# Performance work log

Measured on AMD Instinct MI355X. Metric: run time of the kernel, lower is better.

## Reference

```python
import jax, jax.numpy as jnp
import numpy as np

N, H, CIN, C, G = 50000, 16, 256, 256, 8
CPG = C // G          # 32 channels per group
CR = C // 4           # delta MLP hidden (delta_reduction=4)

def _lrelu(x):
    return jax.nn.leaky_relu(x, 0.1)

def setup_inputs() -> dict:
    key = jax.random.key(0)
    ks = jax.random.split(key, 16)
    def lin(k, fin, fout):
        return jax.random.normal(k, (fin, fout), jnp.float32) / np.sqrt(fin)
    return {
        'q_pts': jax.random.normal(ks[0], (N, 3), jnp.float32),
        's_pts': jax.random.normal(ks[1], (N, 3), jnp.float32),
        's_feats': jax.random.normal(ks[2], (N, CIN), jnp.float32),
        'neighb_inds': jax.random.randint(ks[3], (N, H), 0, N, jnp.int64),
        'Wq': lin(ks[4], CIN, C), 'bq': jnp.zeros((C,), jnp.float32),
        'Wk': lin(ks[5], CIN, C), 'bk': jnp.zeros((C,), jnp.float32),
        'Wv': lin(ks[6], CIN, C), 'bv': jnp.zeros((C,), jnp.float32),
        'Wd1': lin(ks[7], 3, CR), 'bd1': jnp.zeros((CR,), jnp.float32),
        'Wd2': lin(ks[8], CR, C), 'bd2': jnp.zeros((C,), jnp.float32),
        'Wa1': lin(ks[9], C, CPG), 'ba1': jnp.zeros((CPG,), jnp.float32),
        'Wa2': lin(ks[10], CPG, CPG), 'ba2': jnp.zeros((CPG,), jnp.float32),
    }

def reference(q_pts, s_pts, s_feats, neighb_inds,
              Wq, bq, Wk, bk, Wv, bv,
              Wd1, bd1, Wd2, bd2, Wa1, ba1, Wa2, ba2):
    # q/k/v projections  (N, C)
    v = s_feats @ Wv + bv
    k = s_feats @ Wk + bk
    q = s_feats @ Wq + bq
    # gather neighbor features (all indices < N, shadow mask is a no-op)
    nv = v[neighb_inds]                 # (N, H, C)
    nk = k[neighb_inds]                 # (N, H, C)
    # relative positions (torch.no_grad in source)
    rel = s_pts[neighb_inds] - q_pts[:, None, :]   # (N, H, 3)
    # delta MLP: 3 -> C/4 -> C (UnaryBlock + Linear, norm='none')
    geom = _lrelu(rel @ Wd1 + bd1) @ Wd2 + bd2     # (N, H, C)
    # geom_mode='sub': v-branch and qk-branch both subtract geom encodings
    nv = nv - geom
    # source always enters strided branch (s_pts padded before the check);
    # stride_mode='nearest' -> q feature of the first neighbor
    qf = q[neighb_inds[:, 0]]                      # (N, C)
    qk = qf[:, None, :] - nk - geom                # (N, H, C)
    # alpha MLP: NormBlock(id) + act, Linear C->CpG + act, Linear CpG->CpG
    a = _lrelu(qk)
    a = _lrelu(a @ Wa1 + ba1)
    a = a @ Wa2 + ba2                              # (N, H, CpG)
    attn = jax.nn.softmax(a, axis=1)               # softmax over neighbors
    # grouped weighted aggregation: C split as (CpG, G), attn broadcast over G
    out = (nv.reshape(N, H, CPG, G) * attn[..., None]).sum(axis=1)
    return out.reshape(N, C)
```

## Files before the change

kernel.cpp:

```cpp
#include <hip/hip_runtime.h>
#include <cstdint>
#include <cstddef>

#define N_PTS 50000
#define H 16
#define CIN 256
#define C 256
#define CPG 32
#define CR 64

typedef short bf16x8 __attribute__((ext_vector_type(8)));
typedef float f32x4 __attribute__((ext_vector_type(4)));

__device__ __forceinline__ unsigned short f2bf(float f) {
    unsigned int u = __float_as_uint(f);
    u += 0x7fff + ((u >> 16) & 1);
    return (unsigned short)(u >> 16);
}
__device__ __forceinline__ float bf2f(unsigned short s) {
    return __uint_as_float(((unsigned int)s) << 16);
}

__global__ __launch_bounds__(256) void prep_all(
    const float* __restrict__ feats,
    const float* __restrict__ Wq, const float* __restrict__ Wk,
    const float* __restrict__ Wv,
    const float* __restrict__ Wd2, const float* __restrict__ Wa1,
    const float* __restrict__ Wa2,
    unsigned short* __restrict__ A_bf16,
    unsigned short* __restrict__ gemmFrags,
    unsigned short* __restrict__ attnFrags)
{
    int bid = blockIdx.x;
    if (bid < 6250) {
        size_t i = ((size_t)bid * 256 + threadIdx.x) * 8;
        float4 f0 = *(const float4*)&feats[i];
        float4 f1 = *(const float4*)&feats[i + 4];
        unsigned short t[8] = {f2bf(f0.x), f2bf(f0.y), f2bf(f0.z), f2bf(f0.w),
                               f2bf(f1.x), f2bf(f1.y), f2bf(f1.z), f2bf(f1.w)};
        *(bf16x8*)&A_bf16[i] = *(bf16x8*)t;
    } else if (bid < 6346) {
        int t = (bid - 6250) * 256 + threadIdx.x;
        int lane = t & 63;
        int f = t >> 6;
        int ntg = f % 48;
        const float* W = ntg < 16 ? Wq : (ntg < 32 ? Wk : Wv);
        int colc = (ntg & 15) * 16 + (lane & 15);
        int row0 = (f / 48) * 32 + ((lane >> 4) << 3);
        unsigned short tmp[8];
        #pragma unroll
        for (int j = 0; j < 8; ++j) tmp[j] = f2bf(W[(size_t)(row0 + j) * 256 + colc]);
        *(bf16x8*)&gemmFrags[(size_t)t * 8] = *(bf16x8*)tmp;
    } else {
        int t = (bid - 6346) * 256 + threadIdx.x;
        if (t >= 3200) return;
        const float* W; int Nc, NT, loc, base;
        if (t < 2048)      { W = Wd2; Nc = 256; NT = 16; loc = t;        base = 0; }
        else if (t < 3072) { W = Wa1; Nc = 32;  NT = 2;  loc = t - 2048; base = 16384; }
        else               { W = Wa2; Nc = 32;  NT = 2;  loc = t - 3072; base = 24576; }
        int f = loc >> 6, lane = loc & 63;
        int kt = f / NT, nt = f - kt * NT;
        int colc = nt * 16 + (lane & 15);
        int row0 = kt * 32 + ((lane >> 4) << 3);
        unsigned short tmp[8];
        #pragma unroll
        for (int j = 0; j < 8; ++j) tmp[j] = f2bf(W[(size_t)(row0 + j) * Nc + colc]);
        *(bf16x8*)&attnFrags[(size_t)(base + loc * 8)] = *(bf16x8*)tmp;
    }
}

__global__ __launch_bounds__(256) void qkv_gemm_mfma(
    const unsigned short* __restrict__ A,
    const unsigned short* __restrict__ wfrags,
    const float* __restrict__ bq, const float* __restrict__ bk,
    const float* __restrict__ bv, unsigned short* __restrict__ out)
{
    __shared__ unsigned short s_a[128 * 40];
    const int tid = threadIdx.x;
    const int lane = tid & 63, wave = tid >> 6;
    const int quad = lane >> 4, col16 = lane & 15;
    const int bx = blockIdx.x, by = blockIdx.y;

    f32x4 acc[2][8] = {};
    const int mrow = tid >> 1, half = tid & 1;
    const int gm = by * 128 + mrow;

    for (int kt = 0; kt < 8; ++kt) {
        bf16x8 a0 = {0,0,0,0,0,0,0,0}, a1 = a0;
        if (gm < N_PTS) {
            const unsigned short* src = &A[(size_t)gm * 256 + kt * 32 + half * 16];
            a0 = *(const bf16x8*)src;
            a1 = *(const bf16x8*)(src + 8);
        }
        __syncthreads();
        *(bf16x8*)&s_a[mrow * 40 + half * 16]     = a0;
        *(bf16x8*)&s_a[mrow * 40 + half * 16 + 8] = a1;
        __syncthreads();
        bf16x8 af0 = *(bf16x8*)&s_a[(wave * 32 + col16) * 40 + quad * 8];
        bf16x8 af1 = *(bf16x8*)&s_a[(wave * 32 + 16 + col16) * 40 + quad * 8];
        #pragma unroll
        for (int nt = 0; nt < 8; ++nt) {
            bf16x8 bf = *(const bf16x8*)&wfrags[(((size_t)kt * 48 + bx * 8 + nt) * 64 + lane) * 8];
            acc[0][nt] = __builtin_amdgcn_mfma_f32_16x16x32_bf16(af0, bf, acc[0][nt], 0, 0, 0);
            acc[1][nt] = __builtin_amdgcn_mfma_f32_16x16x32_bf16(af1, bf, acc[1][nt], 0, 0, 0);
        }
    }

    const int mode = bx >> 1;
    const float* bias = mode == 0 ? bq : (mode == 1 ? bk : bv);
    #pragma unroll
    for (int nt = 0; nt < 8; ++nt) {
        int cIn = (bx & 1) * 128 + nt * 16 + col16;
        float bb = bias[cIn];
        int pos = mode == 0 ? cIn : (256 + 2 * cIn + (mode == 2 ? 1 : 0));
        #pragma unroll
        for (int mt = 0; mt < 2; ++mt) {
            #pragma unroll
            for (int r = 0; r < 4; ++r) {
                int row = by * 128 + wave * 32 + mt * 16 + quad * 4 + r;
                if (row < N_PTS)
                    out[(size_t)row * 768 + pos] = f2bf(acc[mt][nt][r] + bb);
            }
        }
    }
}

#define D1S 72
#define PGS 66
#define QKS 264
#define A1S 40
#define A2S 33

__global__ __launch_bounds__(256, 3) void attn_mfma(
    const unsigned short* __restrict__ qkv,
    const float* __restrict__ q_pts, const float* __restrict__ s_pts,
    const int* __restrict__ nbr,
    const float* __restrict__ Wd1, const float* __restrict__ bd1,
    const float* __restrict__ bd2,
    const unsigned short* __restrict__ frags,
    const float* __restrict__ ba1, const float* __restrict__ ba2,
    float* __restrict__ out)
{
    __shared__ unsigned short s_d1[H * D1S];
    __shared__ float          s_pg[4 * H * PGS];
    __shared__ unsigned short s_qk[H * QKS];
    __shared__ unsigned short s_a1[H * A1S];
    __shared__ float          s_a2[H * A2S];
    __shared__ float          s_rel[4][H][3];
    __shared__ int            s_idx[4][H];

    const int tid = threadIdx.x;
    const int lane = tid & 63, wave = tid >> 6;
    const int quad = lane >> 4, col = lane & 15;
    const int n0 = blockIdx.x * 4;
    const int c = tid;

    if (tid < 64) {
        int pp = tid >> 4, hh = tid & 15;
        int idx = nbr[(size_t)(n0 + pp) * H + hh];
        s_idx[pp][hh] = idx;
        #pragma unroll
        for (int x = 0; x < 3; ++x)
            s_rel[pp][hh][x] = s_pts[(size_t)idx * 3 + x] - q_pts[(size_t)(n0 + pp) * 3 + x];
    }

    const float w1x = Wd1[lane], w1y = Wd1[64 + lane], w1z = Wd1[128 + lane];
    const float b1 = bd1[lane];
    const float b2 = bd2[c];
    bf16x8 wd2f[2][4];
    #pragma unroll
    for (int t = 0; t < 4; ++t) {
        wd2f[0][t] = *(const bf16x8*)&frags[((size_t)((0 * 16 + wave * 4 + t) * 64 + lane)) * 8];
        wd2f[1][t] = *(const bf16x8*)&frags[((size_t)((1 * 16 + wave * 4 + t) * 64 + lane)) * 8];
    }
    bf16x8 wa1f[8];
    bf16x8 wa2f = {0,0,0,0,0,0,0,0};
    if (wave < 2) {
        #pragma unroll
        for (int kt = 0; kt < 8; ++kt)
            wa1f[kt] = *(const bf16x8*)&frags[16384 + ((size_t)((kt * 2 + wave) * 64 + lane)) * 8];
        wa2f = *(const bf16x8*)&frags[24576 + ((size_t)(wave * 64 + lane)) * 8];
    }
    __syncthreads();

    float* pg = &s_pg[wave * (H * PGS)];

    for (int p = 0; p < 4; ++p) {
        const int n = n0 + p;

        #pragma unroll
        for (int pass = 0; pass < 4; ++pass) {
            int h = pass * 4 + wave;
            float v = b1 + s_rel[p][h][0] * w1x + s_rel[p][h][1] * w1y + s_rel[p][h][2] * w1z;
            s_d1[h * D1S + lane] = f2bf(fmaxf(v, 0.1f * v));
        }
        __syncthreads();

        unsigned int u[H];
        #pragma unroll
        for (int h = 0; h < H; ++h)
            u[h] = *(const unsigned int*)&qkv[(size_t)s_idx[p][h] * 768 + 256 + 2 * c];
        float qf = bf2f(qkv[(size_t)s_idx[p][0] * 768 + c]);

        {
            bf16x8 ga = *(bf16x8*)&s_d1[col * D1S + quad * 8];
            bf16x8 gb = *(bf16x8*)&s_d1[col * D1S + 32 + quad * 8];
            #pragma unroll
            for (int t = 0; t < 4; ++t) {
                f32x4 acc = {0.f, 0.f, 0.f, 0.f};
                acc = __builtin_amdgcn_mfma_f32_16x16x32_bf16(ga, wd2f[0][t], acc, 0, 0, 0);
                acc = __builtin_amdgcn_mfma_f32_16x16x32_bf16(gb, wd2f[1][t], acc, 0, 0, 0);
                #pragma unroll
                for (int rr = 0; rr < 4; ++rr)
                    pg[(quad * 4 + rr) * PGS + t * 16 + col] = acc[rr];
            }
        }

        float vg[H];
        #pragma unroll
        for (int h = 0; h < H; ++h) {
            float g = pg[h * PGS + lane] + b2;
            float nk = __uint_as_float(u[h] << 16);
            float nv = __uint_as_float(u[h] & 0xffff0000u);
            vg[h] = nv - g;
            float tq = qf - nk - g;
            s_qk[h * QKS + c] = f2bf(fmaxf(tq, 0.1f * tq));
        }
        __syncthreads();

        if (wave < 2) {
            f32x4 acc = {0.f, 0.f, 0.f, 0.f};
            #pragma unroll
            for (int kt = 0; kt < 8; ++kt) {
                bf16x8 a = *(bf16x8*)&s_qk[col * QKS + kt * 32 + quad * 8];
                acc = __builtin_amdgcn_mfma_f32_16x16x32_bf16(a, wa1f[kt], acc, 0, 0, 0);
            }
            int j = wave * 16 + col;
            float bb = ba1[j];
            #pragma unroll
            for (int rr = 0; rr < 4; ++rr) {
                float v = acc[rr] + bb;
                s_a1[(quad * 4 + rr) * A1S + j] = f2bf(fmaxf(v, 0.1f * v));
            }
        }
        __syncthreads();

        if (wave < 2) {
            bf16x8 aa = *(bf16x8*)&s_a1[col * A1S + quad * 8];
            f32x4 acc = {0.f, 0.f, 0.f, 0.f};
            acc = __builtin_amdgcn_mfma_f32_16x16x32_bf16(aa, wa2f, acc, 0, 0, 0);
            int j = wave * 16 + col;
            float bb = ba2[j];
            #pragma unroll
            for (int rr = 0; rr < 4; ++rr)
                s_a2[(quad * 4 + rr) * A2S + j] = acc[rr] + bb;
        }
        __syncthreads();

        if (wave == 0) {
            int j = lane & 31, hb = (lane >> 5) * 8;
            float vals[8];
            float mx = -1e30f;
            #pragma unroll
            for (int i = 0; i < 8; ++i) {
                vals[i] = s_a2[(hb + i) * A2S + j];
                mx = fmaxf(mx, vals[i]);
            }
            mx = fmaxf(mx, __shfl_xor(mx, 32));
            float sum = 0.f;
            #pragma unroll
            for (int i = 0; i < 8; ++i) { vals[i] = __expf(vals[i] - mx); sum += vals[i]; }
            sum += __shfl_xor(sum, 32);
            float inv = 1.f / sum;
            #pragma unroll
            for (int i = 0; i < 8; ++i) s_a2[(hb + i) * A2S + j] = vals[i] * inv;
        }
        __syncthreads();

        float o = 0.f;
        const int aj = c >> 3;
        #pragma unroll
        for (int h = 0; h < H; ++h) o += vg[h] * s_a2[h * A2S + aj];
        out[(size_t)n * C + c] = o;
    }
}


extern "C" void kernel_launch(void* const* d_in, const int* in_sizes, int n_in,
                              void* d_out, int out_size, void* d_ws, size_t ws_size,
                              hipStream_t stream) {
    const float* q_pts   = (const float*)d_in[0];
    const float* s_pts   = (const float*)d_in[1];
    const float* s_feats = (const float*)d_in[2];
    const int*   nbr     = (const int*)d_in[3];
    const float* Wq  = (const float*)d_in[4];
    const float* bq  = (const float*)d_in[5];
    const float* Wk  = (const float*)d_in[6];
    const float* bk  = (const float*)d_in[7];
    const float* Wv  = (const float*)d_in[8];
    const float* bv  = (const float*)d_in[9];
    const float* Wd1 = (const float*)d_in[10];
    const float* bd1 = (const float*)d_in[11];
    const float* Wd2 = (const float*)d_in[12];
    const float* bd2 = (const float*)d_in[13];
    const float* Wa1 = (const float*)d_in[14];
    const float* ba1 = (const float*)d_in[15];
    const float* Wa2 = (const float*)d_in[16];
    const float* ba2 = (const float*)d_in[17];

    float* out = (float*)d_out;
    char* ws = (char*)d_ws;
    unsigned short* A_bf16    = (unsigned short*)(ws);
    unsigned short* qkvb      = (unsigned short*)(ws + 25600000);
    unsigned short* attnFrags = (unsigned short*)(ws + 102400000);
    unsigned short* gemmFrags = (unsigned short*)(ws + 102451200);

    prep_all<<<6359, 256, 0, stream>>>(s_feats, Wq, Wk, Wv, Wd2, Wa1, Wa2,
                                       A_bf16, gemmFrags, attnFrags);

    dim3 g1(6, (N_PTS + 127) / 128);
    qkv_gemm_mfma<<<g1, 256, 0, stream>>>(A_bf16, gemmFrags, bq, bk, bv, qkvb);

    attn_mfma<<<(N_PTS / 4), 256, 0, stream>>>(qkvb, q_pts, s_pts, nbr,
                                               Wd1, bd1, bd2, attnFrags,
                                               ba1, ba2, out);
}
```

Before: 404.1 us.

## Double-buffer QKV GEMM loads, prefetch neighbor gathers, and merge alpha MLP stages

The QKV GEMM now double-buffers the A tile in shared memory, prefetching the next k-slice while MFMAs run, and drops one barrier per iteration. K and V columns are interleaved per block so each thread writes packed 32-bit k|v pairs. In the attention kernel, the delta-MLP first layer is computed for all four points up front, the neighbor k/v gathers for the next point are issued before the current softmax/aggregation, and the second alpha layer plus softmax run in a single wave, removing a barrier. This adds register and shared-memory pressure, which may reduce occupancy.

```diff
diff --git a/kernel.cpp b/kernel.cpp
--- a/kernel.cpp
+++ b/kernel.cpp
@@ -75,7 +75,7 @@
     const float* __restrict__ bq, const float* __restrict__ bk,
     const float* __restrict__ bv, unsigned short* __restrict__ out)
 {
-    __shared__ unsigned short s_a[128 * 40];
+    __shared__ unsigned short s_a[2][128 * 40];
     const int tid = threadIdx.x;
     const int lane = tid & 63, wave = tid >> 6;
     const int quad = lane >> 4, col16 = lane & 15;
@@ -84,43 +84,75 @@
     f32x4 acc[2][8] = {};
     const int mrow = tid >> 1, half = tid & 1;
     const int gm = by * 128 + mrow;
-
+    const bool valid = gm < N_PTS;
+    const unsigned short* arow = &A[(size_t)gm * 256 + half * 16];
+
+    {
+        bf16x8 pa0 = {0,0,0,0,0,0,0,0}, pa1 = pa0;
+        if (valid) { pa0 = *(const bf16x8*)arow; pa1 = *(const bf16x8*)(arow + 8); }
+        *(bf16x8*)&s_a[0][mrow * 40 + half * 16]     = pa0;
+        *(bf16x8*)&s_a[0][mrow * 40 + half * 16 + 8] = pa1;
+    }
+
+    #pragma unroll
     for (int kt = 0; kt < 8; ++kt) {
-        bf16x8 a0 = {0,0,0,0,0,0,0,0}, a1 = a0;
-        if (gm < N_PTS) {
-            const unsigned short* src = &A[(size_t)gm * 256 + kt * 32 + half * 16];
-            a0 = *(const bf16x8*)src;
-            a1 = *(const bf16x8*)(src + 8);
+        bf16x8 na0 = {0,0,0,0,0,0,0,0}, na1 = na0;
+        if (kt < 7 && valid) {
+            const unsigned short* src = arow + (kt + 1) * 32;
+            na0 = *(const bf16x8*)src;
+            na1 = *(const bf16x8*)(src + 8);
         }
         __syncthreads();
-        *(bf16x8*)&s_a[mrow * 40 + half * 16]     = a0;
-        *(bf16x8*)&s_a[mrow * 40 + half * 16 + 8] = a1;
-        __syncthreads();
-        bf16x8 af0 = *(bf16x8*)&s_a[(wave * 32 + col16) * 40 + quad * 8];
-        bf16x8 af1 = *(bf16x8*)&s_a[(wave * 32 + 16 + col16) * 40 + quad * 8];
+        const unsigned short* buf = s_a[kt & 1];
+        bf16x8 af0 = *(const bf16x8*)&buf[(wave * 32 + col16) * 40 + quad * 8];
+        bf16x8 af1 = *(const bf16x8*)&buf[(wave * 32 + 16 + col16) * 40 + quad * 8];
         #pragma unroll
         for (int nt = 0; nt < 8; ++nt) {
-            bf16x8 bf = *(const bf16x8*)&wfrags[(((size_t)kt * 48 + bx * 8 + nt) * 64 + lane) * 8];
+            int ntg = (bx < 2) ? (bx * 8 + nt)
+                               : (nt < 4 ? 16 + (bx - 2) * 4 + nt
+                                         : 32 + (bx - 2) * 4 + (nt - 4));
+            bf16x8 bf = *(const bf16x8*)&wfrags[(((size_t)kt * 48 + ntg) * 64 + lane) * 8];
             acc[0][nt] = __builtin_amdgcn_mfma_f32_16x16x32_bf16(af0, bf, acc[0][nt], 0, 0, 0);
             acc[1][nt] = __builtin_amdgcn_mfma_f32_16x16x32_bf16(af1, bf, acc[1][nt], 0, 0, 0);
         }
-    }
-
-    const int mode = bx >> 1;
-    const float* bias = mode == 0 ? bq : (mode == 1 ? bk : bv);
-    #pragma unroll
-    for (int nt = 0; nt < 8; ++nt) {
-        int cIn = (bx & 1) * 128 + nt * 16 + col16;
-        float bb = bias[cIn];
-        int pos = mode == 0 ? cIn : (256 + 2 * cIn + (mode == 2 ? 1 : 0));
-        #pragma unroll
-        for (int mt = 0; mt < 2; ++mt) {
-            #pragma unroll
-            for (int r = 0; r < 4; ++r) {
-                int row = by * 128 + wave * 32 + mt * 16 + quad * 4 + r;
-                if (row < N_PTS)
-                    out[(size_t)row * 768 + pos] = f2bf(acc[mt][nt][r] + bb);
-            }
+        if (kt < 7) {
+            unsigned short* nbuf = s_a[(kt + 1) & 1];
+            *(bf16x8*)&nbuf[mrow * 40 + half * 16]     = na0;
+            *(bf16x8*)&nbuf[mrow * 40 + half * 16 + 8] = na1;
+        }
+    }
+
+    if (bx < 2) {
+        #pragma unroll
+        for (int nt = 0; nt < 8; ++nt) {
+            int cIn = bx * 128 + nt * 16 + col16;
+            float bb = bq[cIn];
+            #pragma unroll
+            for (int mt = 0; mt < 2; ++mt)
+                #pragma unroll
+                for (int r = 0; r < 4; ++r) {
+                    int row = by * 128 + wave * 32 + mt * 16 + quad * 4 + r;
+                    if (row < N_PTS)
+                        out[(size_t)row * 768 + cIn] = f2bf(acc[mt][nt][r] + bb);
+                }
+        }
+    } else {
+        unsigned int* out32 = (unsigned int*)out;
+        #pragma unroll
+        for (int t = 0; t < 4; ++t) {
+            int cIn = (bx - 2) * 64 + t * 16 + col16;
+            float kb = bk[cIn], vb = bv[cIn];
+            #pragma unroll
+            for (int mt = 0; mt < 2; ++mt)
+                #pragma unroll
+                for (int r = 0; r < 4; ++r) {
+                    int row = by * 128 + wave * 32 + mt * 16 + quad * 4 + r;
+                    if (row < N_PTS) {
+                        unsigned int kk = f2bf(acc[mt][t][r] + kb);
+                        unsigned int vv = f2bf(acc[mt][t + 4][r] + vb);
+                        out32[(size_t)row * 384 + 128 + cIn] = kk | (vv << 16);
+                    }
+                }
         }
     }
 }
@@ -141,7 +173,7 @@
     const float* __restrict__ ba1, const float* __restrict__ ba2,
     float* __restrict__ out)
 {
-    __shared__ unsigned short s_d1[H * D1S];
+    __shared__ unsigned short s_d1a[4 * H * D1S];
     __shared__ float          s_pg[4 * H * PGS];
     __shared__ unsigned short s_qk[H * QKS];
     __shared__ unsigned short s_a1[H * A1S];
@@ -174,37 +206,42 @@
         wd2f[1][t] = *(const bf16x8*)&frags[((size_t)((1 * 16 + wave * 4 + t) * 64 + lane)) * 8];
     }
     bf16x8 wa1f[8];
-    bf16x8 wa2f = {0,0,0,0,0,0,0,0};
+    bf16x8 wa2f[2] = {{0,0,0,0,0,0,0,0}, {0,0,0,0,0,0,0,0}};
     if (wave < 2) {
         #pragma unroll
         for (int kt = 0; kt < 8; ++kt)
             wa1f[kt] = *(const bf16x8*)&frags[16384 + ((size_t)((kt * 2 + wave) * 64 + lane)) * 8];
-        wa2f = *(const bf16x8*)&frags[24576 + ((size_t)(wave * 64 + lane)) * 8];
+    }
+    if (wave == 0) {
+        wa2f[0] = *(const bf16x8*)&frags[24576 + ((size_t)(0 * 64 + lane)) * 8];
+        wa2f[1] = *(const bf16x8*)&frags[24576 + ((size_t)(1 * 64 + lane)) * 8];
     }
     __syncthreads();
 
+    #pragma unroll
+    for (int pass = 0; pass < 16; ++pass) {
+        int hp = pass * 4 + wave;
+        int p = hp >> 4, h = hp & 15;
+        float v = b1 + s_rel[p][h][0] * w1x + s_rel[p][h][1] * w1y + s_rel[p][h][2] * w1z;
+        s_d1a[hp * D1S + lane] = f2bf(fmaxf(v, 0.1f * v));
+    }
+    __syncthreads();
+
     float* pg = &s_pg[wave * (H * PGS)];
+
+    unsigned int u[H];
+    #pragma unroll
+    for (int h = 0; h < H; ++h)
+        u[h] = *(const unsigned int*)&qkv[(size_t)s_idx[0][h] * 768 + 256 + 2 * c];
+    float qf = bf2f(qkv[(size_t)s_idx[0][0] * 768 + c]);
 
     for (int p = 0; p < 4; ++p) {
         const int n = n0 + p;
 
-        #pragma unroll
-        for (int pass = 0; pass < 4; ++pass) {
-            int h = pass * 4 + wave;
-            float v = b1 + s_rel[p][h][0] * w1x + s_rel[p][h][1] * w1y + s_rel[p][h][2] * w1z;
-            s_d1[h * D1S + lane] = f2bf(fmaxf(v, 0.1f * v));
-        }
-        __syncthreads();
-
-        unsigned int u[H];
-        #pragma unroll
-        for (int h = 0; h < H; ++h)
-            u[h] = *(const unsigned int*)&qkv[(size_t)s_idx[p][h] * 768 + 256 + 2 * c];
-        float qf = bf2f(qkv[(size_t)s_idx[p][0] * 768 + c]);
-
         {
-            bf16x8 ga = *(bf16x8*)&s_d1[col * D1S + quad * 8];
-            bf16x8 gb = *(bf16x8*)&s_d1[col * D1S + 32 + quad * 8];
+            const unsigned short* d1p = &s_d1a[p * H * D1S];
+            bf16x8 ga = *(const bf16x8*)&d1p[col * D1S + quad * 8];
+            bf16x8 gb = *(const bf16x8*)&d1p[col * D1S + 32 + quad * 8];
             #pragma unroll
             for (int t = 0; t < 4; ++t) {
                 f32x4 acc = {0.f, 0.f, 0.f, 0.f};
@@ -245,19 +282,25 @@
         }
         __syncthreads();
 
-        if (wave < 2) {
+        if (p < 3) {
+            #pragma unroll
+            for (int h = 0; h < H; ++h)
+                u[h] = *(const unsigned int*)&qkv[(size_t)s_idx[p + 1][h] * 768 + 256 + 2 * c];
+            qf = bf2f(qkv[(size_t)s_idx[p + 1][0] * 768 + c]);
+        }
+
+        if (wave == 0) {
             bf16x8 aa = *(bf16x8*)&s_a1[col * A1S + quad * 8];
-            f32x4 acc = {0.f, 0.f, 0.f, 0.f};
-            acc = __builtin_amdgcn_mfma_f32_16x16x32_bf16(aa, wa2f, acc, 0, 0, 0);
-            int j = wave * 16 + col;
-            float bb = ba2[j];
-            #pragma unroll
-            for (int rr = 0; rr < 4; ++rr)
-                s_a2[(quad * 4 + rr) * A2S + j] = acc[rr] + bb;
-        }
-        __syncthreads();
-
-        if (wave == 0) {
+            #pragma unroll
+            for (int nt = 0; nt < 2; ++nt) {
+                f32x4 acc = {0.f, 0.f, 0.f, 0.f};
+                acc = __builtin_amdgcn_mfma_f32_16x16x32_bf16(aa, wa2f[nt], acc, 0, 0, 0);
+                int j = nt * 16 + col;
+                float bb = ba2[j];
+                #pragma unroll
+                for (int rr = 0; rr < 4; ++rr)
+                    s_a2[(quad * 4 + rr) * A2S + j] = acc[rr] + bb;
+            }
             int j = lane & 31, hb = (lane >> 5) * 8;
             float vals[8];
             float mx = -1e30f;
```

After: 417.8 us. 1.03x slower.
